# Performance work log

Hardware: AMD Instinct MI355X
Metric: run time of the kernel (lower is better)

The kernel has to match this reference:

```python
import jax, jax.numpy as jnp
import numpy as np

B = 8192        # batch of spots
T = 137         # target_length: number of predict heads
D = 384         # fea_size(256) + img_size(128)
K = 128         # hidden width of each head
EPS = 1e-5      # BatchNorm1d eps
SLOPE = 0.01    # LeakyReLU negative slope (torch default)


def setup_inputs() -> dict:
    key = jax.random.key(0)
    ks = jax.random.split(key, 5)
    return {
        "f":        jax.random.normal(ks[0], (B, D), dtype=jnp.float32),
        "W1":       jax.random.normal(ks[1], (T, K, D), dtype=jnp.float32) * (1.0 / np.sqrt(D)),
        "b1":       jax.random.normal(ks[2], (T, K), dtype=jnp.float32) * 0.02,
        "gamma":    jnp.ones((T, K), dtype=jnp.float32),
        "beta":     jnp.zeros((T, K), dtype=jnp.float32),
        "run_mean": jnp.zeros((T, K), dtype=jnp.float32),
        "run_var":  jnp.ones((T, K), dtype=jnp.float32),
        "W2":       jax.random.normal(ks[3], (T, K), dtype=jnp.float32) * (1.0 / np.sqrt(K)),
        "b2":       jax.random.normal(ks[4], (T,), dtype=jnp.float32) * 0.02,
    }


def reference(f, W1, b1, gamma, beta, run_mean, run_var, W2, b2):
    # Batched equivalent of: for i in range(137): Linear(384->128)+BN+LeakyReLU+Linear(128->1)
    # all applied to the same feature f; outputs concatenated -> [B, 137].
    h = jnp.einsum('bd,tkd->btk', f, W1) + b1                       # [B, T, K]
    scale = gamma * jax.lax.rsqrt(run_var + EPS)                     # eval-mode BN, [T, K]
    h = (h - run_mean) * scale + beta
    h = jnp.where(h >= 0, h, SLOPE * h)                              # LeakyReLU
    out = jnp.einsum('btk,tk->bt', h, W2) + b2                       # [B, T]
    return out
```

## Files before the change

kernel.cpp:

```cpp
#include <hip/hip_runtime.h>
#include <hip/hip_bf16.h>

constexpr int BATCH = 8192;
constexpr int THEADS = 137;
constexpr int DFEA = 384;
constexpr int KHID = 128;
constexpr float EPS_BN = 1e-5f;
constexpr float SLOPE = 0.01f;

constexpr size_t N_F  = (size_t)BATCH * DFEA;
constexpr size_t N_W1 = (size_t)THEADS * KHID * DFEA;
constexpr size_t WS_NEED = (N_F + N_W1) * sizeof(__hip_bfloat16);
constexpr int C_F8 = (int)(N_F / 8);
constexpr int C_T8 = (int)((N_F + N_W1) / 8);

typedef __attribute__((ext_vector_type(8))) short bf16x8;
typedef __attribute__((ext_vector_type(4))) float f32x4;

__device__ __forceinline__ short cvt_bf16(float x) {
    __hip_bfloat16 b = __float2bfloat16(x);
    return *(short*)&b;
}

__device__ __forceinline__ bf16x8 load8_cvt(const float* __restrict__ g) {
    f32x4 lo = *(const f32x4*)g;
    f32x4 hi = *(const f32x4*)(g + 4);
    bf16x8 r;
    r[0] = cvt_bf16(lo[0]); r[1] = cvt_bf16(lo[1]);
    r[2] = cvt_bf16(lo[2]); r[3] = cvt_bf16(lo[3]);
    r[4] = cvt_bf16(hi[0]); r[5] = cvt_bf16(hi[1]);
    r[6] = cvt_bf16(hi[2]); r[7] = cvt_bf16(hi[3]);
    return r;
}

__device__ __forceinline__ void gload16(const void* g, void* s) {
    __builtin_amdgcn_global_load_lds((const __attribute__((address_space(1))) void*)g,
                                     (__attribute__((address_space(3))) void*)s,
                                     16, 0, 0);
}

__global__ __launch_bounds__(256) void cvt_pass(const float* __restrict__ f,
                                                const float* __restrict__ W1,
                                                __hip_bfloat16* __restrict__ ws) {
    int i = blockIdx.x * 256 + threadIdx.x;
    if (i < C_F8)
        *(bf16x8*)(ws + (size_t)i * 8) = load8_cvt(f + (size_t)i * 8);
    else if (i < C_T8)
        *(bf16x8*)(ws + (size_t)i * 8) = load8_cvt(W1 + ((size_t)i - C_F8) * 8);
}

__global__ __launch_bounds__(256, 2) void fused_heads_v8(
    const __hip_bfloat16* __restrict__ fb,
    const __hip_bfloat16* __restrict__ W1b,
    const float* __restrict__ b1,
    const float* __restrict__ gmm,
    const float* __restrict__ bta,
    const float* __restrict__ rmean,
    const float* __restrict__ rvar,
    const float* __restrict__ W2,
    const float* __restrict__ b2,
    float* __restrict__ out)
{
    __shared__ __attribute__((aligned(16))) __hip_bfloat16 As[3][256 * 32];
    __shared__ __attribute__((aligned(16))) __hip_bfloat16 Bs[3][128 * 32];

    const int tid  = threadIdx.x;
    const int lane = tid & 63;
    const int wm   = tid >> 6;
    const int m0 = blockIdx.x * 256;
    const int t  = blockIdx.y;
    const int n0 = t * KHID;

    const int row16 = lane & 15;
    const int quad  = lane >> 4;
    const int swz   = quad ^ ((row16 >> 1) & 3);

    const __hip_bfloat16* gA[4];
    const __hip_bfloat16* gB[2];
    #pragma unroll
    for (int c = 0; c < 4; ++c) {
        const int li = tid + c * 256;
        const int r = li >> 2, cb = (li & 3) ^ ((li >> 3) & 3);
        gA[c] = fb + (size_t)(m0 + r) * DFEA + cb * 8;
    }
    #pragma unroll
    for (int c = 0; c < 2; ++c) {
        const int li = tid + c * 256;
        const int r = li >> 2, cb = (li & 3) ^ ((li >> 3) & 3);
        gB[c] = W1b + (size_t)(n0 + r) * DFEA + cb * 8;
    }

    f32x4 acc[4][8];
    #pragma unroll
    for (int i = 0; i < 4; ++i)
        #pragma unroll
        for (int j = 0; j < 8; ++j)
            acc[i][j] = (f32x4){0.f, 0.f, 0.f, 0.f};

#define STAGE(BUF, K0)                                                      \
    {                                                                       \
        _Pragma("unroll")                                                   \
        for (int c = 0; c < 4; ++c)                                         \
            gload16(gA[c] + (K0), &As[BUF][(tid + c * 256) * 8]);           \
        _Pragma("unroll")                                                   \
        for (int c = 0; c < 2; ++c)                                         \
            gload16(gB[c] + (K0), &Bs[BUF][(tid + c * 256) * 8]);           \
    }

    STAGE(0, 0);
    STAGE(1, 32);

#define KSTEP(KT, CUR, STG)                                                   \
    {                                                                         \
        if ((KT) < 11) { asm volatile("s_waitcnt vmcnt(6)" ::: "memory"); }   \
        else           { asm volatile("s_waitcnt vmcnt(0)" ::: "memory"); }   \
        __builtin_amdgcn_s_barrier();            \
        __builtin_amdgcn_sched_barrier(0);       \
        if ((KT) < 10) STAGE(STG, ((KT) + 2) * 32);                           \
        bf16x8 af[4], bfr[8];                                                 \
        _Pragma("unroll")                                                     \
        for (int ai = 0; ai < 4; ++ai)                                        \
            af[ai] = *(const bf16x8*)&As[CUR][(wm * 64 + ai * 16 + row16) * 32 + swz * 8]; \
        _Pragma("unroll")                                                     \
        for (int bi = 0; bi < 8; ++bi)                                        \
            bfr[bi] = *(const bf16x8*)&Bs[CUR][(bi * 16 + row16) * 32 + swz * 8]; \
        __builtin_amdgcn_s_setprio(1);                                        \
        _Pragma("unroll")                                                     \
        for (int ai = 0; ai < 4; ++ai)                                        \
            _Pragma("unroll")                                                 \
            for (int bi = 0; bi < 8; ++bi)                                    \
                acc[ai][bi] = __builtin_amdgcn_mfma_f32_16x16x32_bf16(        \
                    af[ai], bfr[bi], acc[ai][bi], 0, 0, 0);                   \
        __builtin_amdgcn_s_setprio(0);                                        \
    }

    #pragma unroll
    for (int kp = 0; kp < 4; ++kp) {
        KSTEP(3 * kp,     0, 2)
        KSTEP(3 * kp + 1, 1, 0)
        KSTEP(3 * kp + 2, 2, 1)
    }
#undef KSTEP
#undef STAGE

    float s[8], cc[8], w2v[8];
    #pragma unroll
    for (int bi = 0; bi < 8; ++bi) {
        const int n = n0 + bi * 16 + row16;
        const float sv = gmm[n] * rsqrtf(rvar[n] + EPS_BN);
        s[bi]   = sv;
        cc[bi]  = bta[n] + (b1[n] - rmean[n]) * sv;
        w2v[bi] = W2[n];
    }

    float p[4][4];
    #pragma unroll
    for (int ai = 0; ai < 4; ++ai)
        #pragma unroll
        for (int r = 0; r < 4; ++r) {
            float a = 0.f;
            #pragma unroll
            for (int bi = 0; bi < 8; ++bi) {
                float y = acc[ai][bi][r] * s[bi] + cc[bi];
                y = (y >= 0.f) ? y : SLOPE * y;
                a += y * w2v[bi];
            }
            p[ai][r] = a;
        }

    #pragma unroll
    for (int mask = 1; mask <= 8; mask <<= 1)
        #pragma unroll
        for (int ai = 0; ai < 4; ++ai)
            #pragma unroll
            for (int r = 0; r < 4; ++r)
                p[ai][r] += __shfl_xor(p[ai][r], mask);

    if (row16 == 0) {
        const float bias = b2[t];
        #pragma unroll
        for (int ai = 0; ai < 4; ++ai)
            #pragma unroll
            for (int r = 0; r < 4; ++r) {
                const int row = m0 + wm * 64 + ai * 16 + quad * 4 + r;
                out[(size_t)row * THEADS + t] = p[ai][r] + bias;
            }
    }
}

__global__ __launch_bounds__(256) void fused_heads_f32(
    const float* __restrict__ f, const float* __restrict__ W1,
    const float* __restrict__ b1, const float* __restrict__ gmm,
    const float* __restrict__ bta, const float* __restrict__ rmean,
    const float* __restrict__ rvar, const float* __restrict__ W2,
    const float* __restrict__ b2, float* __restrict__ out)
{
    __shared__ __attribute__((aligned(16))) __hip_bfloat16 As[128 * 32];
    __shared__ __attribute__((aligned(16))) __hip_bfloat16 Bs[128 * 32];
    __shared__ float red[2][128];

    const int tid  = threadIdx.x;
    const int lane = tid & 63;
    const int wave = tid >> 6;
    const int wmv = wave >> 1, wn = wave & 1;
    const int m0 = blockIdx.x * 128;
    const int t  = blockIdx.y;
    const int n0 = t * KHID;

    const int li0 = tid, li1 = tid + 256;
    const int r0 = li0 >> 2, c0 = (li0 & 3) * 8;
    const int r1 = li1 >> 2, c1 = (li1 & 3) * 8;
    const float* gA0 = f  + (size_t)(m0 + r0) * DFEA + c0;
    const float* gA1 = f  + (size_t)(m0 + r1) * DFEA + c1;
    const float* gB0 = W1 + (size_t)(n0 + r0) * DFEA + c0;
    const float* gB1 = W1 + (size_t)(n0 + r1) * DFEA + c1;

    const int row16 = lane & 15, quad = lane >> 4;

    f32x4 acc[4][4];
    #pragma unroll
    for (int i = 0; i < 4; ++i)
        #pragma unroll
        for (int jx = 0; jx < 4; ++jx)
            acc[i][jx] = (f32x4){0.f, 0.f, 0.f, 0.f};

    #pragma unroll 1
    for (int kt = 0; kt < DFEA / 32; ++kt) {
        const int k0 = kt * 32;
        bf16x8 va0 = load8_cvt(gA0 + k0);
        bf16x8 va1 = load8_cvt(gA1 + k0);
        bf16x8 vb0 = load8_cvt(gB0 + k0);
        bf16x8 vb1 = load8_cvt(gB1 + k0);
        __syncthreads();
        *(bf16x8*)&As[li0 * 8] = va0;
        *(bf16x8*)&As[li1 * 8] = va1;
        *(bf16x8*)&Bs[li0 * 8] = vb0;
        *(bf16x8*)&Bs[li1 * 8] = vb1;
        __syncthreads();

        bf16x8 af[4], bfr[4];
        #pragma unroll
        for (int i = 0; i < 4; ++i)
            af[i] = *(const bf16x8*)&As[(wmv * 64 + i * 16 + row16) * 32 + quad * 8];
        #pragma unroll
        for (int i = 0; i < 4; ++i)
            bfr[i] = *(const bf16x8*)&Bs[(wn * 64 + i * 16 + row16) * 32 + quad * 8];
        #pragma unroll
        for (int ai = 0; ai < 4; ++ai)
            #pragma unroll
            for (int bi = 0; bi < 4; ++bi)
                acc[ai][bi] = __builtin_amdgcn_mfma_f32_16x16x32_bf16(
                    af[ai], bfr[bi], acc[ai][bi], 0, 0, 0);
    }

    float s[4], cc[4], w2v[4];
    #pragma unroll
    for (int bi = 0; bi < 4; ++bi) {
        const int n = n0 + wn * 64 + bi * 16 + row16;
        const float sv = gmm[n] * rsqrtf(rvar[n] + EPS_BN);
        s[bi] = sv;
        cc[bi] = bta[n] + (b1[n] - rmean[n]) * sv;
        w2v[bi] = W2[n];
    }
    float p[4][4];
    #pragma unroll
    for (int ai = 0; ai < 4; ++ai)
        #pragma unroll
        for (int r = 0; r < 4; ++r) {
            float a = 0.f;
            #pragma unroll
            for (int bi = 0; bi < 4; ++bi) {
                float y = acc[ai][bi][r] * s[bi] + cc[bi];
                y = (y >= 0.f) ? y : SLOPE * y;
                a += y * w2v[bi];
            }
            p[ai][r] = a;
        }
    #pragma unroll
    for (int mask = 1; mask <= 8; mask <<= 1)
        #pragma unroll
        for (int ai = 0; ai < 4; ++ai)
            #pragma unroll
            for (int r = 0; r < 4; ++r)
                p[ai][r] += __shfl_xor(p[ai][r], mask);
    if (row16 == 0) {
        #pragma unroll
        for (int ai = 0; ai < 4; ++ai)
            #pragma unroll
            for (int r = 0; r < 4; ++r)
                red[wn][wmv * 64 + ai * 16 + quad * 4 + r] = p[ai][r];
    }
    __syncthreads();
    if (tid < 128)
        out[(size_t)(m0 + tid) * THEADS + t] = red[0][tid] + red[1][tid] + b2[t];
}

extern "C" void kernel_launch(void* const* d_in, const int* in_sizes, int n_in,
                              void* d_out, int out_size, void* d_ws, size_t ws_size,
                              hipStream_t stream) {
    (void)in_sizes; (void)n_in; (void)out_size;
    const float* f     = (const float*)d_in[0];
    const float* W1    = (const float*)d_in[1];
    const float* b1    = (const float*)d_in[2];
    const float* gmm   = (const float*)d_in[3];
    const float* bta   = (const float*)d_in[4];
    const float* rmean = (const float*)d_in[5];
    const float* rvar  = (const float*)d_in[6];
    const float* W2    = (const float*)d_in[7];
    const float* b2    = (const float*)d_in[8];
    float* out = (float*)d_out;

    if (ws_size >= WS_NEED) {
        __hip_bfloat16* fb  = (__hip_bfloat16*)d_ws;
        __hip_bfloat16* W1b = fb + N_F;
        cvt_pass<<<(C_T8 + 255) / 256, 256, 0, stream>>>(f, W1, fb);
        dim3 grid(BATCH / 256, THEADS);
        fused_heads_v8<<<grid, 256, 0, stream>>>(fb, W1b, b1, gmm, bta, rmean, rvar, W2, b2, out);
    } else {
        dim3 grid(BATCH / 128, THEADS);
        fused_heads_f32<<<grid, 256, 0, stream>>>(f, W1, b1, gmm, bta, rmean, rvar, W2, b2, out);
    }
}
```

Before: 221.5 us.

## Shrink M tile to 128 with 2x2 wave grid and LDS cross-wave reduction

Cuts the block tile from 256x128 to 128x128 and arranges the four waves as a 2x2 grid, each computing a 64x64 sub-tile. The two column-half partial sums of the second linear layer are combined through a small shared-memory buffer before writing the output. Halving the accumulator count and the A staging buffer lowers register and LDS pressure, and launch bounds now target 3 blocks per CU with twice as many blocks in the grid. In exchange each block reuses the loaded W1 tile over fewer rows, so global and LDS traffic per MFMA goes up, and an extra barrier is added before the store.

```diff
diff --git a/kernel.cpp b/kernel.cpp
--- a/kernel.cpp
+++ b/kernel.cpp
@@ -49,7 +49,7 @@
         *(bf16x8*)(ws + (size_t)i * 8) = load8_cvt(W1 + ((size_t)i - C_F8) * 8);
 }
 
-__global__ __launch_bounds__(256, 2) void fused_heads_v8(
+__global__ __launch_bounds__(256, 3) void fused_heads_v9(
     const __hip_bfloat16* __restrict__ fb,
     const __hip_bfloat16* __restrict__ W1b,
     const float* __restrict__ b1,
@@ -61,13 +61,16 @@
     const float* __restrict__ b2,
     float* __restrict__ out)
 {
-    __shared__ __attribute__((aligned(16))) __hip_bfloat16 As[3][256 * 32];
+    __shared__ __attribute__((aligned(16))) __hip_bfloat16 As[3][128 * 32];
     __shared__ __attribute__((aligned(16))) __hip_bfloat16 Bs[3][128 * 32];
+    __shared__ float red[2][128];
 
     const int tid  = threadIdx.x;
     const int lane = tid & 63;
-    const int wm   = tid >> 6;
-    const int m0 = blockIdx.x * 256;
+    const int wave = tid >> 6;
+    const int wr   = wave >> 1;
+    const int wc   = wave & 1;
+    const int m0 = blockIdx.x * 128;
     const int t  = blockIdx.y;
     const int n0 = t * KHID;
 
@@ -75,32 +78,27 @@
     const int quad  = lane >> 4;
     const int swz   = quad ^ ((row16 >> 1) & 3);
 
-    const __hip_bfloat16* gA[4];
+    const __hip_bfloat16* gA[2];
     const __hip_bfloat16* gB[2];
-    #pragma unroll
-    for (int c = 0; c < 4; ++c) {
-        const int li = tid + c * 256;
-        const int r = li >> 2, cb = (li & 3) ^ ((li >> 3) & 3);
-        gA[c] = fb + (size_t)(m0 + r) * DFEA + cb * 8;
-    }
     #pragma unroll
     for (int c = 0; c < 2; ++c) {
         const int li = tid + c * 256;
         const int r = li >> 2, cb = (li & 3) ^ ((li >> 3) & 3);
+        gA[c] = fb  + (size_t)(m0 + r) * DFEA + cb * 8;
         gB[c] = W1b + (size_t)(n0 + r) * DFEA + cb * 8;
     }
 
-    f32x4 acc[4][8];
+    f32x4 acc[4][4];
     #pragma unroll
     for (int i = 0; i < 4; ++i)
         #pragma unroll
-        for (int j = 0; j < 8; ++j)
+        for (int j = 0; j < 4; ++j)
             acc[i][j] = (f32x4){0.f, 0.f, 0.f, 0.f};
 
 #define STAGE(BUF, K0)                                                      \
     {                                                                       \
         _Pragma("unroll")                                                   \
-        for (int c = 0; c < 4; ++c)                                         \
+        for (int c = 0; c < 2; ++c)                                         \
             gload16(gA[c] + (K0), &As[BUF][(tid + c * 256) * 8]);           \
         _Pragma("unroll")                                                   \
         for (int c = 0; c < 2; ++c)                                         \
@@ -112,23 +110,23 @@
 
 #define KSTEP(KT, CUR, STG)                                                   \
     {                                                                         \
-        if ((KT) < 11) { asm volatile("s_waitcnt vmcnt(6)" ::: "memory"); }   \
+        if ((KT) < 11) { asm volatile("s_waitcnt vmcnt(4)" ::: "memory"); }   \
         else           { asm volatile("s_waitcnt vmcnt(0)" ::: "memory"); }   \
-        __builtin_amdgcn_s_barrier();            \
-        __builtin_amdgcn_sched_barrier(0);       \
+        __builtin_amdgcn_s_barrier();                                         \
+        __builtin_amdgcn_sched_barrier(0);                                    \
         if ((KT) < 10) STAGE(STG, ((KT) + 2) * 32);                           \
-        bf16x8 af[4], bfr[8];                                                 \
+        bf16x8 af[4], bfr[4];                                                 \
         _Pragma("unroll")                                                     \
         for (int ai = 0; ai < 4; ++ai)                                        \
-            af[ai] = *(const bf16x8*)&As[CUR][(wm * 64 + ai * 16 + row16) * 32 + swz * 8]; \
+            af[ai] = *(const bf16x8*)&As[CUR][(wr * 64 + ai * 16 + row16) * 32 + swz * 8]; \
         _Pragma("unroll")                                                     \
-        for (int bi = 0; bi < 8; ++bi)                                        \
-            bfr[bi] = *(const bf16x8*)&Bs[CUR][(bi * 16 + row16) * 32 + swz * 8]; \
+        for (int bi = 0; bi < 4; ++bi)                                        \
+            bfr[bi] = *(const bf16x8*)&Bs[CUR][(wc * 64 + bi * 16 + row16) * 32 + swz * 8]; \
         __builtin_amdgcn_s_setprio(1);                                        \
         _Pragma("unroll")                                                     \
         for (int ai = 0; ai < 4; ++ai)                                        \
             _Pragma("unroll")                                                 \
-            for (int bi = 0; bi < 8; ++bi)                                    \
+            for (int bi = 0; bi < 4; ++bi)                                    \
                 acc[ai][bi] = __builtin_amdgcn_mfma_f32_16x16x32_bf16(        \
                     af[ai], bfr[bi], acc[ai][bi], 0, 0, 0);                   \
         __builtin_amdgcn_s_setprio(0);                                        \
@@ -143,10 +141,10 @@
 #undef KSTEP
 #undef STAGE
 
-    float s[8], cc[8], w2v[8];
-    #pragma unroll
-    for (int bi = 0; bi < 8; ++bi) {
-        const int n = n0 + bi * 16 + row16;
+    float s[4], cc[4], w2v[4];
+    #pragma unroll
+    for (int bi = 0; bi < 4; ++bi) {
+        const int n = n0 + wc * 64 + bi * 16 + row16;
         const float sv = gmm[n] * rsqrtf(rvar[n] + EPS_BN);
         s[bi]   = sv;
         cc[bi]  = bta[n] + (b1[n] - rmean[n]) * sv;
@@ -160,7 +158,7 @@
         for (int r = 0; r < 4; ++r) {
             float a = 0.f;
             #pragma unroll
-            for (int bi = 0; bi < 8; ++bi) {
+            for (int bi = 0; bi < 4; ++bi) {
                 float y = acc[ai][bi][r] * s[bi] + cc[bi];
                 y = (y >= 0.f) ? y : SLOPE * y;
                 a += y * w2v[bi];
@@ -177,15 +175,15 @@
                 p[ai][r] += __shfl_xor(p[ai][r], mask);
 
     if (row16 == 0) {
-        const float bias = b2[t];
-        #pragma unroll
-        for (int ai = 0; ai < 4; ++ai)
-            #pragma unroll
-            for (int r = 0; r < 4; ++r) {
-                const int row = m0 + wm * 64 + ai * 16 + quad * 4 + r;
-                out[(size_t)row * THEADS + t] = p[ai][r] + bias;
-            }
-    }
+        #pragma unroll
+        for (int ai = 0; ai < 4; ++ai)
+            #pragma unroll
+            for (int r = 0; r < 4; ++r)
+                red[wc][wr * 64 + ai * 16 + quad * 4 + r] = p[ai][r];
+    }
+    __syncthreads();
+    if (tid < 128)
+        out[(size_t)(m0 + tid) * THEADS + t] = red[0][tid] + red[1][tid] + b2[t];
 }
 
 __global__ __launch_bounds__(256) void fused_heads_f32(
@@ -314,8 +312,8 @@
         __hip_bfloat16* fb  = (__hip_bfloat16*)d_ws;
         __hip_bfloat16* W1b = fb + N_F;
         cvt_pass<<<(C_T8 + 255) / 256, 256, 0, stream>>>(f, W1, fb);
-        dim3 grid(BATCH / 256, THEADS);
-        fused_heads_v8<<<grid, 256, 0, stream>>>(fb, W1b, b1, gmm, bta, rmean, rvar, W2, b2, out);
+        dim3 grid(BATCH / 128, THEADS);
+        fused_heads_v9<<<grid, 256, 0, stream>>>(fb, W1b, b1, gmm, bta, rmean, rvar, W2, b2, out);
     } else {
         dim3 grid(BATCH / 128, THEADS);
         fused_heads_f32<<<grid, 256, 0, stream>>>(f, W1, b1, gmm, bta, rmean, rvar, W2, b2, out);
```

New measurement: 236.3 us. 6.7% more time.

## Stage W1 in two large halves and give each wave private A buffers

Applied to the files above, without the earlier changes.

Each wave now loads its own 64-row A slice into a per-wave double buffer. This removes the block-wide barrier on every k-step. The B tile (weights) is staged in two halves of six k-slices each, so only two block barriers remain. The aim is to cut synchronisation overhead and let waves run out of step while keeping MFMA fed. The cost is larger shared memory (6 B buffers plus per-wave A buffers). There is also a stall at the halfway point, where all of B must be reloaded before the second half of the k-loop can start.

```diff
diff --git a/kernel.cpp b/kernel.cpp
--- a/kernel.cpp
+++ b/kernel.cpp
@@ -49,7 +49,7 @@
         *(bf16x8*)(ws + (size_t)i * 8) = load8_cvt(W1 + ((size_t)i - C_F8) * 8);
 }
 
-__global__ __launch_bounds__(256, 2) void fused_heads_v8(
+__global__ __launch_bounds__(256, 2) void fused_heads_v10(
     const __hip_bfloat16* __restrict__ fb,
     const __hip_bfloat16* __restrict__ W1b,
     const float* __restrict__ b1,
@@ -61,34 +61,45 @@
     const float* __restrict__ b2,
     float* __restrict__ out)
 {
-    __shared__ __attribute__((aligned(16))) __hip_bfloat16 As[3][256 * 32];
-    __shared__ __attribute__((aligned(16))) __hip_bfloat16 Bs[3][128 * 32];
-
-    const int tid  = threadIdx.x;
-    const int lane = tid & 63;
-    const int wm   = tid >> 6;
+    __shared__ __attribute__((aligned(16))) __hip_bfloat16 Bs[6][128 * 32];
+    __shared__ __attribute__((aligned(16))) __hip_bfloat16 As[4][2][64 * 32];
+
+    const int tid   = threadIdx.x;
+    const int lane  = tid & 63;
+    const int wm    = tid >> 6;
+    const int row16 = lane & 15;
+    const int quad  = lane >> 4;
     const int m0 = blockIdx.x * 256;
     const int t  = blockIdx.y;
     const int n0 = t * KHID;
 
-    const int row16 = lane & 15;
-    const int quad  = lane >> 4;
-    const int swz   = quad ^ ((row16 >> 1) & 3);
-
-    const __hip_bfloat16* gA[4];
+    const int swz = quad ^ ((row16 >> 1) & 3);
+
     const __hip_bfloat16* gB[2];
-    #pragma unroll
-    for (int c = 0; c < 4; ++c) {
-        const int li = tid + c * 256;
-        const int r = li >> 2, cb = (li & 3) ^ ((li >> 3) & 3);
-        gA[c] = fb + (size_t)(m0 + r) * DFEA + cb * 8;
-    }
     #pragma unroll
     for (int c = 0; c < 2; ++c) {
         const int li = tid + c * 256;
         const int r = li >> 2, cb = (li & 3) ^ ((li >> 3) & 3);
         gB[c] = W1b + (size_t)(n0 + r) * DFEA + cb * 8;
     }
+#define STAGEB_HALF(H)                                                        \
+    { _Pragma("unroll")                                                       \
+      for (int j = 0; j < 6; ++j)                                             \
+          _Pragma("unroll")                                                   \
+          for (int c = 0; c < 2; ++c)                                         \
+              gload16(gB[c] + (H) * 192 + j * 32, &Bs[j][(tid + c * 256) * 8]); }
+
+    const __hip_bfloat16* gA[4];
+    #pragma unroll
+    for (int c = 0; c < 4; ++c) {
+        const int li = lane + c * 64;
+        const int r = li >> 2, cb = (li & 3) ^ ((li >> 3) & 3);
+        gA[c] = fb + (size_t)(m0 + wm * 64 + r) * DFEA + cb * 8;
+    }
+#define STAGEA(BUF, K0)                                                       \
+    { _Pragma("unroll")                                                       \
+      for (int c = 0; c < 4; ++c)                                             \
+          gload16(gA[c] + (K0), &As[wm][BUF][(lane + c * 64) * 8]); }
 
     f32x4 acc[4][8];
     #pragma unroll
@@ -97,33 +108,26 @@
         for (int j = 0; j < 8; ++j)
             acc[i][j] = (f32x4){0.f, 0.f, 0.f, 0.f};
 
-#define STAGE(BUF, K0)                                                      \
-    {                                                                       \
-        _Pragma("unroll")                                                   \
-        for (int c = 0; c < 4; ++c)                                         \
-            gload16(gA[c] + (K0), &As[BUF][(tid + c * 256) * 8]);           \
-        _Pragma("unroll")                                                   \
-        for (int c = 0; c < 2; ++c)                                         \
-            gload16(gB[c] + (K0), &Bs[BUF][(tid + c * 256) * 8]);           \
-    }
-
-    STAGE(0, 0);
-    STAGE(1, 32);
-
-#define KSTEP(KT, CUR, STG)                                                   \
+    STAGEB_HALF(0);
+    STAGEA(0, 0);
+    STAGEA(1, 32);
+    asm volatile("s_waitcnt vmcnt(4)" ::: "memory");
+    __builtin_amdgcn_s_barrier();
+
+#define KSTEP(KT)                                                             \
     {                                                                         \
-        if ((KT) < 11) { asm volatile("s_waitcnt vmcnt(6)" ::: "memory"); }   \
-        else           { asm volatile("s_waitcnt vmcnt(0)" ::: "memory"); }   \
-        __builtin_amdgcn_s_barrier();            \
-        __builtin_amdgcn_sched_barrier(0);       \
-        if ((KT) < 10) STAGE(STG, ((KT) + 2) * 32);                           \
+        if ((KT) == 11) { asm volatile("s_waitcnt vmcnt(0)" ::: "memory"); }  \
+        else            { asm volatile("s_waitcnt vmcnt(4)" ::: "memory"); }  \
         bf16x8 af[4], bfr[8];                                                 \
         _Pragma("unroll")                                                     \
         for (int ai = 0; ai < 4; ++ai)                                        \
-            af[ai] = *(const bf16x8*)&As[CUR][(wm * 64 + ai * 16 + row16) * 32 + swz * 8]; \
+            af[ai] = *(const bf16x8*)&As[wm][(KT) & 1][(ai * 16 + row16) * 32 + swz * 8]; \
+        asm volatile("s_waitcnt lgkmcnt(0)" ::: "memory");                    \
+        __builtin_amdgcn_sched_barrier(0);                                    \
+        if ((KT) < 10 && (KT) != 5) STAGEA((KT) & 1, ((KT) + 2) * 32);        \
         _Pragma("unroll")                                                     \
         for (int bi = 0; bi < 8; ++bi)                                        \
-            bfr[bi] = *(const bf16x8*)&Bs[CUR][(bi * 16 + row16) * 32 + swz * 8]; \
+            bfr[bi] = *(const bf16x8*)&Bs[(KT) % 6][(bi * 16 + row16) * 32 + swz * 8]; \
         __builtin_amdgcn_s_setprio(1);                                        \
         _Pragma("unroll")                                                     \
         for (int ai = 0; ai < 4; ++ai)                                        \
@@ -134,14 +138,18 @@
         __builtin_amdgcn_s_setprio(0);                                        \
     }
 
-    #pragma unroll
-    for (int kp = 0; kp < 4; ++kp) {
-        KSTEP(3 * kp,     0, 2)
-        KSTEP(3 * kp + 1, 1, 0)
-        KSTEP(3 * kp + 2, 2, 1)
-    }
+    KSTEP(0) KSTEP(1) KSTEP(2) KSTEP(3) KSTEP(4) KSTEP(5)
+
+    __builtin_amdgcn_s_barrier();
+    STAGEB_HALF(1);
+    STAGEA(1, 7 * 32);
+    asm volatile("s_waitcnt vmcnt(0)" ::: "memory");
+    __builtin_amdgcn_s_barrier();
+
+    KSTEP(6) KSTEP(7) KSTEP(8) KSTEP(9) KSTEP(10) KSTEP(11)
 #undef KSTEP
-#undef STAGE
+#undef STAGEA
+#undef STAGEB_HALF
 
     float s[8], cc[8], w2v[8];
     #pragma unroll
@@ -315,7 +323,7 @@
         __hip_bfloat16* W1b = fb + N_F;
         cvt_pass<<<(C_T8 + 255) / 256, 256, 0, stream>>>(f, W1, fb);
         dim3 grid(BATCH / 256, THEADS);
-        fused_heads_v8<<<grid, 256, 0, stream>>>(fb, W1b, b1, gmm, bta, rmean, rvar, W2, b2, out);
+        fused_heads_v10<<<grid, 256, 0, stream>>>(fb, W1b, b1, gmm, bta, rmean, rvar, W2, b2, out);
     } else {
         dim3 grid(BATCH / 128, THEADS);
         fused_heads_f32<<<grid, 256, 0, stream>>>(f, W1, b1, gmm, bta, rmean, rvar, W2, b2, out);
```

Result: faster. 207.9 us (-6.2%).
